# Kernel tuning notes

Measured on AMD Instinct MI355X. Metric: run time of the kernel, lower is better.

The kernel has to match this reference:

```python
import jax, jax.numpy as jnp
import numpy as np

N_ITEMS = 100000
EMBED_DIM = 128
N_SESSIONS = 16384
TOTAL_ITEMS = 819200


def setup_inputs() -> dict:
    key = jax.random.key(0)
    k1, k2, k3 = jax.random.split(key, 3)
    embeddings = jax.random.normal(k1, (N_ITEMS, EMBED_DIM), dtype=jnp.float32)
    item_ids = jax.random.randint(k2, (TOTAL_ITEMS,), 0, N_ITEMS, dtype=jnp.int64)
    segment_ids = jnp.sort(jax.random.randint(k3, (TOTAL_ITEMS,), 0, N_SESSIONS, dtype=jnp.int64))
    return {"embeddings": embeddings, "item_ids": item_ids,
            "segment_ids": segment_ids, "num_sessions": N_SESSIONS}


def reference(embeddings, item_ids, segment_ids, num_sessions):
    # Ragged per-session mean of gathered item embeddings
    gathered = embeddings[item_ids]                      # [total_items, d]
    sums = jax.ops.segment_sum(gathered, segment_ids, num_segments=num_sessions)
    counts = jax.ops.segment_sum(jnp.ones((item_ids.shape[0],), dtype=embeddings.dtype),
                                 segment_ids, num_segments=num_sessions)
    counts = jnp.maximum(counts, 1.0)                    # guard empty sessions
    return sums / counts[:, None]                        # [num_sessions, d]
```

## Files before the change

### kernel.cpp

```cpp
#include <hip/hip_runtime.h>
#include <hip/hip_fp16.h>


constexpr int D = 128;
constexpr int IDS_CAP = 4096;

typedef float f32x2 __attribute__((ext_vector_type(2)));
typedef float f32x4 __attribute__((ext_vector_type(4)));
typedef unsigned int u32x2 __attribute__((ext_vector_type(2)));

__global__ __launch_bounds__(256)
void prep_kernel(const float* __restrict__ emb, __half* __restrict__ emb2,
                 const int* __restrict__ seg, int* __restrict__ starts,
                 int nitems, int total, int nsess, int repack_blocks) {
    if ((int)blockIdx.x < repack_blocks) {
        const int item = blockIdx.x * 4 + (threadIdx.x >> 6);
        if (item >= nitems) return;
        const int lane = threadIdx.x & 63;
        const f32x2 v = __builtin_nontemporal_load(
            reinterpret_cast<const f32x2*>(emb + (size_t)item * D) + lane);
        const __half2 h = __floats2half2_rn(v.x, v.y);
        const int g = lane >> 4;
        const int o = lane & 15;
        __half2* dst = reinterpret_cast<__half2*>(
            emb2 + (size_t)g * nitems * 32 + (size_t)item * 32);
        dst[o] = h;
    } else {
        const int j = ((int)blockIdx.x - repack_blocks) * 256 + threadIdx.x;
        if (j >= total) return;
        const int cur  = seg[j];
        const int prev = (j == 0) ? -1 : seg[j - 1];
        for (int s = prev + 1; s <= cur; ++s) starts[s] = j;
        if (j == total - 1) {
            for (int s = cur + 1; s <= nsess; ++s) starts[s] = total;
        }
    }
}

__global__ __launch_bounds__(256)
void gather_mean_half(const __half* __restrict__ emb2,
                      const int* __restrict__ ids,
                      const int* __restrict__ starts,
                      float* __restrict__ partial,
                      int nitems, int nsess) {
    __shared__ int lds_off[IDS_CAP];

    const int key  = blockIdx.x & 7;
    const int g    = key & 3;
    const int h    = key >> 2;
    const int s0   = (blockIdx.x >> 3) * 32;
    const int sidx = s0 + (threadIdx.x >> 3);
    const int dl   = threadIdx.x & 7;

    const int sEnd  = (s0 + 32 < nsess) ? s0 + 32 : nsess;
    const int base0 = starts[s0];
    const int range = starts[sEnd] - base0;
    const bool use_lds = (range <= IDS_CAP);

    if (use_lds) {
        for (int t = threadIdx.x; t < range; t += 256)
            lds_off[t] = ids[base0 + t] << 6;
    }
    __syncthreads();

    if (sidx >= nsess) return;

    const int beg = starts[sidx];
    const int len = starts[sidx + 1] - beg;
    const int hb  = (nitems >> 1) << 6;

    const char* pbase = reinterpret_cast<const char*>(emb2)
                      + (size_t)g * nitems * 64 + dl * 8;

    float a0 = 0.f, a1 = 0.f, a2 = 0.f, a3 = 0.f;

    if (use_lds) {
        const int* offp = lds_off + (beg - base0);
        int j = 0;
        for (; j + 8 <= len; j += 8) {
            u32x2 r[8];
            #pragma unroll
            for (int k = 0; k < 8; ++k) {
                const int off = offp[j + k];
                const bool take = h ? (off >= hb) : (off < hb);
                r[k].x = 0u; r[k].y = 0u;
                if (take)
                    r[k] = *reinterpret_cast<const u32x2*>(pbase + (size_t)off);
            }
            #pragma unroll
            for (int k = 0; k < 8; ++k) {
                unsigned lo = r[k].x, hi = r[k].y;
                const float2 f0 = __half22float2(*reinterpret_cast<const __half2*>(&lo));
                const float2 f1 = __half22float2(*reinterpret_cast<const __half2*>(&hi));
                a0 += f0.x; a1 += f0.y; a2 += f1.x; a3 += f1.y;
            }
        }
        for (; j < len; ++j) {
            const int off = offp[j];
            const bool take = h ? (off >= hb) : (off < hb);
            if (take) {
                const u32x2 r = *reinterpret_cast<const u32x2*>(pbase + (size_t)off);
                unsigned lo = r.x, hi = r.y;
                const float2 f0 = __half22float2(*reinterpret_cast<const __half2*>(&lo));
                const float2 f1 = __half22float2(*reinterpret_cast<const __half2*>(&hi));
                a0 += f0.x; a1 += f0.y; a2 += f1.x; a3 += f1.y;
            }
        }
    } else {
        const int* idp = ids + beg;
        for (int j = 0; j < len; ++j) {
            const int off = idp[j] << 6;
            const bool take = h ? (off >= hb) : (off < hb);
            if (take) {
                const u32x2 r = *reinterpret_cast<const u32x2*>(pbase + (size_t)off);
                unsigned lo = r.x, hi = r.y;
                const float2 f0 = __half22float2(*reinterpret_cast<const __half2*>(&lo));
                const float2 f1 = __half22float2(*reinterpret_cast<const __half2*>(&hi));
                a0 += f0.x; a1 += f0.y; a2 += f1.x; a3 += f1.y;
            }
        }
    }

    const float inv = (len > 0) ? 1.0f / (float)len : 0.0f;
    f32x4 o = {a0 * inv, a1 * inv, a2 * inv, a3 * inv};
    float* dst = partial + (size_t)h * nsess * D + (size_t)sidx * D
               + g * 32 + dl * 4;
    __builtin_nontemporal_store(o, reinterpret_cast<f32x4*>(dst));
}

__global__ __launch_bounds__(256)
void combine_kernel(const float* __restrict__ partial, float* __restrict__ out,
                    int n4) {
    const int i = blockIdx.x * 256 + threadIdx.x;
    if (i >= n4) return;
    const f32x4 a = __builtin_nontemporal_load(
        reinterpret_cast<const f32x4*>(partial) + i);
    const f32x4 b = __builtin_nontemporal_load(
        reinterpret_cast<const f32x4*>(partial) + n4 + i);
    f32x4 o = {a.x + b.x, a.y + b.y, a.z + b.z, a.w + b.w};
    reinterpret_cast<f32x4*>(out)[i] = o;
}

__global__ __launch_bounds__(256)
void gather_mean_g4(const __half* __restrict__ emb2,
                    const int* __restrict__ ids,
                    const int* __restrict__ starts,
                    float* __restrict__ out,
                    int nitems, int nsess) {
    __shared__ int lds_off[IDS_CAP];

    const int g    = blockIdx.x & 3;
    const int s0   = (blockIdx.x >> 2) * 32;
    const int sidx = s0 + (threadIdx.x >> 3);
    const int dl   = threadIdx.x & 7;

    const int sEnd  = (s0 + 32 < nsess) ? s0 + 32 : nsess;
    const int base0 = starts[s0];
    const int range = starts[sEnd] - base0;
    const bool use_lds = (range <= IDS_CAP);

    if (use_lds) {
        for (int t = threadIdx.x; t < range; t += 256)
            lds_off[t] = ids[base0 + t] << 6;
    }
    __syncthreads();

    if (sidx >= nsess) return;

    const int beg = starts[sidx];
    const int len = starts[sidx + 1] - beg;

    const char* pbase = reinterpret_cast<const char*>(emb2)
                      + (size_t)g * nitems * 64 + dl * 8;

    float a0 = 0.f, a1 = 0.f, a2 = 0.f, a3 = 0.f;

    if (use_lds) {
        const int* offp = lds_off + (beg - base0);
        int j = 0;
        for (; j + 8 <= len; j += 8) {
            int off[8];
            #pragma unroll
            for (int k = 0; k < 8; ++k) off[k] = offp[j + k];
            u32x2 r[8];
            #pragma unroll
            for (int k = 0; k < 8; ++k)
                r[k] = *reinterpret_cast<const u32x2*>(pbase + (size_t)off[k]);
            #pragma unroll
            for (int k = 0; k < 8; ++k) {
                unsigned lo = r[k].x, hi = r[k].y;
                const float2 f0 = __half22float2(*reinterpret_cast<const __half2*>(&lo));
                const float2 f1 = __half22float2(*reinterpret_cast<const __half2*>(&hi));
                a0 += f0.x; a1 += f0.y; a2 += f1.x; a3 += f1.y;
            }
        }
        for (; j < len; ++j) {
            const u32x2 r = *reinterpret_cast<const u32x2*>(pbase + (size_t)offp[j]);
            unsigned lo = r.x, hi = r.y;
            const float2 f0 = __half22float2(*reinterpret_cast<const __half2*>(&lo));
            const float2 f1 = __half22float2(*reinterpret_cast<const __half2*>(&hi));
            a0 += f0.x; a1 += f0.y; a2 += f1.x; a3 += f1.y;
        }
    } else {
        const int* idp = ids + beg;
        for (int j = 0; j < len; ++j) {
            const u32x2 r = *reinterpret_cast<const u32x2*>(
                pbase + ((size_t)idp[j] << 6));
            unsigned lo = r.x, hi = r.y;
            const float2 f0 = __half22float2(*reinterpret_cast<const __half2*>(&lo));
            const float2 f1 = __half22float2(*reinterpret_cast<const __half2*>(&hi));
            a0 += f0.x; a1 += f0.y; a2 += f1.x; a3 += f1.y;
        }
    }

    const float inv = (len > 0) ? 1.0f / (float)len : 0.0f;
    f32x4 o = {a0 * inv, a1 * inv, a2 * inv, a3 * inv};
    *reinterpret_cast<f32x4*>(out + (size_t)sidx * D + g * 32 + dl * 4) = o;
}

__global__ void find_starts_diff(const int* __restrict__ seg, int total,
                                 int nsess, int* __restrict__ starts) {
    int j = blockIdx.x * blockDim.x + threadIdx.x;
    if (j >= total) return;
    const int cur  = seg[j];
    const int prev = (j == 0) ? -1 : seg[j - 1];
    for (int s = prev + 1; s <= cur; ++s) starts[s] = j;
    if (j == total - 1) {
        for (int s = cur + 1; s <= nsess; ++s) starts[s] = total;
    }
}

__global__ __launch_bounds__(256)
void seg_mean_kernel(const float* __restrict__ emb,
                     const int* __restrict__ ids,
                     const int* __restrict__ starts,
                     float* __restrict__ out, int nsess) {
    const int tid  = threadIdx.x;
    const int s    = blockIdx.x * 4 + (tid >> 6);
    if (s >= nsess) return;
    const int lane = tid & 63;
    const int gq   = lane >> 5;
    const int l32  = lane & 31;

    const int beg = starts[s];
    const int end = starts[s + 1];

    float4 acc = make_float4(0.f, 0.f, 0.f, 0.f);
    for (int j = beg + gq; j < end; j += 2) {
        const int id = ids[j];
        const float4 v = reinterpret_cast<const float4*>(emb + (size_t)id * D)[l32];
        acc.x += v.x; acc.y += v.y; acc.z += v.z; acc.w += v.w;
    }
    acc.x += __shfl_down(acc.x, 32);
    acc.y += __shfl_down(acc.y, 32);
    acc.z += __shfl_down(acc.z, 32);
    acc.w += __shfl_down(acc.w, 32);
    if (lane < 32) {
        const int cnt = end - beg;
        const float inv = (cnt > 0) ? 1.0f / (float)cnt : 0.0f;
        const float4 o = make_float4(acc.x * inv, acc.y * inv,
                                     acc.z * inv, acc.w * inv);
        reinterpret_cast<float4*>(out + (size_t)s * D)[l32] = o;
    }
}

extern "C" void kernel_launch(void* const* d_in, const int* in_sizes, int n_in,
                              void* d_out, int out_size, void* d_ws, size_t ws_size,
                              hipStream_t stream) {
    const float* emb = (const float*)d_in[0];
    const int*   ids = (const int*)d_in[1];
    const int*   seg = (const int*)d_in[2];
    float*       out = (float*)d_out;

    const int total  = in_sizes[1];
    const int nsess  = out_size / D;
    const int nitems = in_sizes[0] / D;

    const size_t emb2_bytes   = (size_t)nitems * D * 2;
    const size_t emb2_pad     = (emb2_bytes + 255) & ~(size_t)255;
    const size_t starts_bytes = (size_t)(nsess + 1) * 4;
    const size_t starts_pad   = (starts_bytes + 255) & ~(size_t)255;
    const size_t partial_bytes = (size_t)2 * nsess * D * 4;
    const size_t need_full = emb2_pad + starts_pad + partial_bytes;
    const size_t need_mid  = emb2_pad + starts_bytes;

    if (ws_size >= need_full) {
        __half* emb2    = (__half*)d_ws;
        int*    starts  = (int*)((char*)d_ws + emb2_pad);
        float*  partial = (float*)((char*)d_ws + emb2_pad + starts_pad);

        const int repack_blocks = (nitems + 3) / 4;
        const int starts_blocks = (total + 255) / 256;
        prep_kernel<<<repack_blocks + starts_blocks, 256, 0, stream>>>(
            emb, emb2, seg, starts, nitems, total, nsess, repack_blocks);

        const int sgroups = (nsess + 31) / 32;
        gather_mean_half<<<sgroups * 8, 256, 0, stream>>>(emb2, ids, starts,
                                                          partial, nitems, nsess);

        const int n4 = nsess * (D / 4);
        combine_kernel<<<(n4 + 255) / 256, 256, 0, stream>>>(partial, out, n4);
    } else if (ws_size >= need_mid) {
        __half* emb2   = (__half*)d_ws;
        int*    starts = (int*)((char*)d_ws + emb2_pad);

        const int repack_blocks = (nitems + 3) / 4;
        const int starts_blocks = (total + 255) / 256;
        prep_kernel<<<repack_blocks + starts_blocks, 256, 0, stream>>>(
            emb, emb2, seg, starts, nitems, total, nsess, repack_blocks);

        const int sgroups = (nsess + 31) / 32;
        gather_mean_g4<<<sgroups * 4, 256, 0, stream>>>(emb2, ids, starts,
                                                        out, nitems, nsess);
    } else {
        int* starts = (int*)d_ws;
        const int blocks = (total + 255) / 256;
        find_starts_diff<<<blocks, 256, 0, stream>>>(seg, total, nsess, starts);
        const int sblocks = (nsess + 3) / 4;
        seg_mean_kernel<<<sblocks, 256, 0, stream>>>(emb, ids, starts, out, nsess);
    }
}
```

Measured before the change: 65.95 us.

## Pre-partition session item ids by table half so gather skips predicated lanes

Session starts are now found per session by binary search over the sorted segment ids instead of one thread per item. Each session thread also splits its item ids into low-half and high-half lists, storing pre-shifted offsets in a new ids2 buffer with a per-session midpoint. The gather kernel then walks only the ids that belong to its table half, dropping the per-item compare and the wasted predicated slots. The cost is a serial per-session scan of about 50 ids in the prep kernel across only about 16K threads, plus extra workspace and global writes.

```diff
diff --git a/kernel.cpp b/kernel.cpp
--- a/kernel.cpp
+++ b/kernel.cpp
@@ -11,8 +11,11 @@
 
 __global__ __launch_bounds__(256)
 void prep_kernel(const float* __restrict__ emb, __half* __restrict__ emb2,
-                 const int* __restrict__ seg, int* __restrict__ starts,
-                 int nitems, int total, int nsess, int repack_blocks) {
+                 const int* __restrict__ seg, const int* __restrict__ ids,
+                 int* __restrict__ ids2, int* __restrict__ starts,
+                 int* __restrict__ mid,
+                 int nitems, int total, int nsess, int repack_blocks,
+                 int do_part) {
     if ((int)blockIdx.x < repack_blocks) {
         const int item = blockIdx.x * 4 + (threadIdx.x >> 6);
         if (item >= nitems) return;
@@ -26,28 +29,42 @@
             emb2 + (size_t)g * nitems * 32 + (size_t)item * 32);
         dst[o] = h;
     } else {
-        const int j = ((int)blockIdx.x - repack_blocks) * 256 + threadIdx.x;
-        if (j >= total) return;
-        const int cur  = seg[j];
-        const int prev = (j == 0) ? -1 : seg[j - 1];
-        for (int s = prev + 1; s <= cur; ++s) starts[s] = j;
-        if (j == total - 1) {
-            for (int s = cur + 1; s <= nsess; ++s) starts[s] = total;
-        }
-    }
-}
-
-__global__ __launch_bounds__(256)
-void gather_mean_half(const __half* __restrict__ emb2,
-                      const int* __restrict__ ids,
+        const int s = ((int)blockIdx.x - repack_blocks) * 256 + threadIdx.x;
+        if (s > nsess) return;
+        int lo = 0, hi = total;
+        while (lo < hi) { const int m = (lo + hi) >> 1;
+                          if (seg[m] < s) lo = m + 1; else hi = m; }
+        starts[s] = lo;
+        if (!do_part || s == nsess) return;
+        int lo2 = lo, hi2 = total;
+        while (lo2 < hi2) { const int m = (lo2 + hi2) >> 1;
+                            if (seg[m] < s + 1) lo2 = m + 1; else hi2 = m; }
+        const int e = lo2;
+        const int half = nitems >> 1;
+        int nlow = 0;
+        for (int j = lo; j < e; ++j) nlow += (ids[j] < half) ? 1 : 0;
+        mid[s] = lo + nlow;
+        int c0 = lo, c1 = lo + nlow;
+        for (int j = lo; j < e; ++j) {
+            const int id = ids[j];
+            if (id < half) ids2[c0++] = id << 6;
+            else           ids2[c1++] = id << 6;
+        }
+    }
+}
+
+__global__ __launch_bounds__(256)
+void gather_mean_part(const __half* __restrict__ emb2,
+                      const int* __restrict__ ids2,
                       const int* __restrict__ starts,
+                      const int* __restrict__ mid,
                       float* __restrict__ partial,
                       int nitems, int nsess) {
     __shared__ int lds_off[IDS_CAP];
 
     const int key  = blockIdx.x & 7;
     const int g    = key & 3;
-    const int h    = key >> 2;
+    const int hh   = key >> 2;
     const int s0   = (blockIdx.x >> 3) * 32;
     const int sidx = s0 + (threadIdx.x >> 3);
     const int dl   = threadIdx.x & 7;
@@ -59,15 +76,19 @@
 
     if (use_lds) {
         for (int t = threadIdx.x; t < range; t += 256)
-            lds_off[t] = ids[base0 + t] << 6;
+            lds_off[t] = ids2[base0 + t];
     }
     __syncthreads();
 
     if (sidx >= nsess) return;
 
-    const int beg = starts[sidx];
-    const int len = starts[sidx + 1] - beg;
-    const int hb  = (nitems >> 1) << 6;
+    const int lo  = starts[sidx];
+    const int hix = starts[sidx + 1];
+    const int m   = mid[sidx];
+    const int b   = hh ? m : lo;
+    const int e   = hh ? hix : m;
+    const int lenh = e - b;
+    const int flen = hix - lo;
 
     const char* pbase = reinterpret_cast<const char*>(emb2)
                       + (size_t)g * nitems * 64 + dl * 8;
@@ -75,55 +96,45 @@
     float a0 = 0.f, a1 = 0.f, a2 = 0.f, a3 = 0.f;
 
     if (use_lds) {
-        const int* offp = lds_off + (beg - base0);
+        const int* offp = lds_off + (b - base0);
         int j = 0;
-        for (; j + 8 <= len; j += 8) {
+        for (; j + 8 <= lenh; j += 8) {
+            int off[8];
+            #pragma unroll
+            for (int k = 0; k < 8; ++k) off[k] = offp[j + k];
             u32x2 r[8];
             #pragma unroll
+            for (int k = 0; k < 8; ++k)
+                r[k] = *reinterpret_cast<const u32x2*>(pbase + (size_t)off[k]);
+            #pragma unroll
             for (int k = 0; k < 8; ++k) {
-                const int off = offp[j + k];
-                const bool take = h ? (off >= hb) : (off < hb);
-                r[k].x = 0u; r[k].y = 0u;
-                if (take)
-                    r[k] = *reinterpret_cast<const u32x2*>(pbase + (size_t)off);
-            }
-            #pragma unroll
-            for (int k = 0; k < 8; ++k) {
-                unsigned lo = r[k].x, hi = r[k].y;
-                const float2 f0 = __half22float2(*reinterpret_cast<const __half2*>(&lo));
-                const float2 f1 = __half22float2(*reinterpret_cast<const __half2*>(&hi));
+                unsigned lov = r[k].x, hiv = r[k].y;
+                const float2 f0 = __half22float2(*reinterpret_cast<const __half2*>(&lov));
+                const float2 f1 = __half22float2(*reinterpret_cast<const __half2*>(&hiv));
                 a0 += f0.x; a1 += f0.y; a2 += f1.x; a3 += f1.y;
             }
         }
-        for (; j < len; ++j) {
-            const int off = offp[j];
-            const bool take = h ? (off >= hb) : (off < hb);
-            if (take) {
-                const u32x2 r = *reinterpret_cast<const u32x2*>(pbase + (size_t)off);
-                unsigned lo = r.x, hi = r.y;
-                const float2 f0 = __half22float2(*reinterpret_cast<const __half2*>(&lo));
-                const float2 f1 = __half22float2(*reinterpret_cast<const __half2*>(&hi));
-                a0 += f0.x; a1 += f0.y; a2 += f1.x; a3 += f1.y;
-            }
+        for (; j < lenh; ++j) {
+            const u32x2 r = *reinterpret_cast<const u32x2*>(pbase + (size_t)offp[j]);
+            unsigned lov = r.x, hiv = r.y;
+            const float2 f0 = __half22float2(*reinterpret_cast<const __half2*>(&lov));
+            const float2 f1 = __half22float2(*reinterpret_cast<const __half2*>(&hiv));
+            a0 += f0.x; a1 += f0.y; a2 += f1.x; a3 += f1.y;
         }
     } else {
-        const int* idp = ids + beg;
-        for (int j = 0; j < len; ++j) {
-            const int off = idp[j] << 6;
-            const bool take = h ? (off >= hb) : (off < hb);
-            if (take) {
-                const u32x2 r = *reinterpret_cast<const u32x2*>(pbase + (size_t)off);
-                unsigned lo = r.x, hi = r.y;
-                const float2 f0 = __half22float2(*reinterpret_cast<const __half2*>(&lo));
-                const float2 f1 = __half22float2(*reinterpret_cast<const __half2*>(&hi));
-                a0 += f0.x; a1 += f0.y; a2 += f1.x; a3 += f1.y;
-            }
-        }
-    }
-
-    const float inv = (len > 0) ? 1.0f / (float)len : 0.0f;
+        const int* offp = ids2 + b;
+        for (int j = 0; j < lenh; ++j) {
+            const u32x2 r = *reinterpret_cast<const u32x2*>(pbase + (size_t)offp[j]);
+            unsigned lov = r.x, hiv = r.y;
+            const float2 f0 = __half22float2(*reinterpret_cast<const __half2*>(&lov));
+            const float2 f1 = __half22float2(*reinterpret_cast<const __half2*>(&hiv));
+            a0 += f0.x; a1 += f0.y; a2 += f1.x; a3 += f1.y;
+        }
+    }
+
+    const float inv = (flen > 0) ? 1.0f / (float)flen : 0.0f;
     f32x4 o = {a0 * inv, a1 * inv, a2 * inv, a3 * inv};
-    float* dst = partial + (size_t)h * nsess * D + (size_t)sidx * D
+    float* dst = partial + (size_t)hh * nsess * D + (size_t)sidx * D
                + g * 32 + dl * 4;
     __builtin_nontemporal_store(o, reinterpret_cast<f32x4*>(dst));
 }
@@ -188,17 +199,17 @@
                 r[k] = *reinterpret_cast<const u32x2*>(pbase + (size_t)off[k]);
             #pragma unroll
             for (int k = 0; k < 8; ++k) {
-                unsigned lo = r[k].x, hi = r[k].y;
-                const float2 f0 = __half22float2(*reinterpret_cast<const __half2*>(&lo));
-                const float2 f1 = __half22float2(*reinterpret_cast<const __half2*>(&hi));
+                unsigned lov = r[k].x, hiv = r[k].y;
+                const float2 f0 = __half22float2(*reinterpret_cast<const __half2*>(&lov));
+                const float2 f1 = __half22float2(*reinterpret_cast<const __half2*>(&hiv));
                 a0 += f0.x; a1 += f0.y; a2 += f1.x; a3 += f1.y;
             }
         }
         for (; j < len; ++j) {
             const u32x2 r = *reinterpret_cast<const u32x2*>(pbase + (size_t)offp[j]);
-            unsigned lo = r.x, hi = r.y;
-            const float2 f0 = __half22float2(*reinterpret_cast<const __half2*>(&lo));
-            const float2 f1 = __half22float2(*reinterpret_cast<const __half2*>(&hi));
+            unsigned lov = r.x, hiv = r.y;
+            const float2 f0 = __half22float2(*reinterpret_cast<const __half2*>(&lov));
+            const float2 f1 = __half22float2(*reinterpret_cast<const __half2*>(&hiv));
             a0 += f0.x; a1 += f0.y; a2 += f1.x; a3 += f1.y;
         }
     } else {
@@ -206,9 +217,9 @@
         for (int j = 0; j < len; ++j) {
             const u32x2 r = *reinterpret_cast<const u32x2*>(
                 pbase + ((size_t)idp[j] << 6));
-            unsigned lo = r.x, hi = r.y;
-            const float2 f0 = __half22float2(*reinterpret_cast<const __half2*>(&lo));
-            const float2 f1 = __half22float2(*reinterpret_cast<const __half2*>(&hi));
+            unsigned lov = r.x, hiv = r.y;
+            const float2 f0 = __half22float2(*reinterpret_cast<const __half2*>(&lov));
+            const float2 f1 = __half22float2(*reinterpret_cast<const __half2*>(&hiv));
             a0 += f0.x; a1 += f0.y; a2 += f1.x; a3 += f1.y;
         }
     }
@@ -276,27 +287,33 @@
     const int nsess  = out_size / D;
     const int nitems = in_sizes[0] / D;
 
-    const size_t emb2_bytes   = (size_t)nitems * D * 2;
-    const size_t emb2_pad     = (emb2_bytes + 255) & ~(size_t)255;
-    const size_t starts_bytes = (size_t)(nsess + 1) * 4;
-    const size_t starts_pad   = (starts_bytes + 255) & ~(size_t)255;
-    const size_t partial_bytes = (size_t)2 * nsess * D * 4;
-    const size_t need_full = emb2_pad + starts_pad + partial_bytes;
-    const size_t need_mid  = emb2_pad + starts_bytes;
+    auto pad = [](size_t x) { return (x + 255) & ~(size_t)255; };
+    const size_t emb2_pad    = pad((size_t)nitems * D * 2);
+    const size_t ids2_pad    = pad((size_t)total * 4);
+    const size_t starts_pad  = pad((size_t)(nsess + 1) * 4);
+    const size_t mid_pad     = pad((size_t)nsess * 4);
+    const size_t partial_sz  = (size_t)2 * nsess * D * 4;
+    const size_t need_full   = emb2_pad + ids2_pad + starts_pad + mid_pad + partial_sz;
+    const size_t need_mid    = emb2_pad + (size_t)(nsess + 1) * 4;
+
+    const int repack_blocks = (nitems + 3) / 4;
+    const int sess_blocks   = (nsess + 1 + 255) / 256;
 
     if (ws_size >= need_full) {
-        __half* emb2    = (__half*)d_ws;
-        int*    starts  = (int*)((char*)d_ws + emb2_pad);
-        float*  partial = (float*)((char*)d_ws + emb2_pad + starts_pad);
-
-        const int repack_blocks = (nitems + 3) / 4;
-        const int starts_blocks = (total + 255) / 256;
-        prep_kernel<<<repack_blocks + starts_blocks, 256, 0, stream>>>(
-            emb, emb2, seg, starts, nitems, total, nsess, repack_blocks);
+        char* w = (char*)d_ws;
+        __half* emb2    = (__half*)w;                  w += emb2_pad;
+        int*    ids2    = (int*)w;                     w += ids2_pad;
+        int*    starts  = (int*)w;                     w += starts_pad;
+        int*    midp    = (int*)w;                     w += mid_pad;
+        float*  partial = (float*)w;
+
+        prep_kernel<<<repack_blocks + sess_blocks, 256, 0, stream>>>(
+            emb, emb2, seg, ids, ids2, starts, midp,
+            nitems, total, nsess, repack_blocks, 1);
 
         const int sgroups = (nsess + 31) / 32;
-        gather_mean_half<<<sgroups * 8, 256, 0, stream>>>(emb2, ids, starts,
-                                                          partial, nitems, nsess);
+        gather_mean_part<<<sgroups * 8, 256, 0, stream>>>(
+            emb2, ids2, starts, midp, partial, nitems, nsess);
 
         const int n4 = nsess * (D / 4);
         combine_kernel<<<(n4 + 255) / 256, 256, 0, stream>>>(partial, out, n4);
@@ -304,10 +321,9 @@
         __half* emb2   = (__half*)d_ws;
         int*    starts = (int*)((char*)d_ws + emb2_pad);
 
-        const int repack_blocks = (nitems + 3) / 4;
-        const int starts_blocks = (total + 255) / 256;
-        prep_kernel<<<repack_blocks + starts_blocks, 256, 0, stream>>>(
-            emb, emb2, seg, starts, nitems, total, nsess, repack_blocks);
+        prep_kernel<<<repack_blocks + sess_blocks, 256, 0, stream>>>(
+            emb, emb2, seg, ids, nullptr, starts, nullptr,
+            nitems, total, nsess, repack_blocks, 0);
 
         const int sgroups = (nsess + 31) / 32;
         gather_mean_g4<<<sgroups * 4, 256, 0, stream>>>(emb2, ids, starts,
```

New measurement: 102.7 us. +55.8%, slower.
